# Performance work log

Hardware: AMD Instinct MI355X
Metric: run time of the kernel (lower is better)

The kernel has to match this reference:

```python
import jax, jax.numpy as jnp
import numpy as np

R = 0.01          # slice width (init kwarg r)
DIM = 0           # init kwarg dim = 'x'
NUM_SLICES = 101  # static bound: coords ~ U[0,1) so ceil(range/R) <= 100; +1 safety


def setup_inputs() -> dict:
    key = jax.random.key(0)
    k1, k2 = jax.random.split(key)
    B, N = 16, 65536
    x = jax.random.uniform(k1, (B, 3, N), dtype=jnp.float32)      # point coords in [0,1)
    x_64 = jax.random.normal(k2, (B, 64, N), dtype=jnp.float32)   # per-point features
    return {"x": x, "x_64": x_64, "batch_": B, "points": N}


def reference(x, x_64, batch_, points):
    # per-batch min along the chosen axis: [B]
    pmin = x[:, DIM, :].min(axis=1)
    coord = x[:, DIM, :]                                          # [B, N]
    # bucket index per point (torch.floor((point - min)/r))
    k = jnp.floor((coord - pmin[:, None]) / R).astype(jnp.int32)  # [B, N]
    seg = k.reshape(-1)                                           # [B*N] global slice ids (original pools across batch)
    feats = jnp.transpose(x_64, (0, 2, 1)).reshape(-1, 64)        # [B*N, 64]
    # vectorized segment max replacing the python per-slice loop
    max_feature = jax.ops.segment_max(feats, seg, num_segments=NUM_SLICES)  # [NUM_SLICES, 64]
    counts = jax.ops.segment_sum(jnp.ones_like(seg, dtype=jnp.int32), seg,
                                 num_segments=NUM_SLICES)         # [NUM_SLICES] = slice_num
    return max_feature, counts
```

## Files before the change

### kernel.cpp

```cpp
#include <hip/hip_runtime.h>

#define NSEG 101
#define NCH 64
#define NPTS 65536
#define NBATCH 16
#define NMAX (NCH * NSEG)
#define NOUT (NMAX + NSEG)
#define FLT_BIG 3.4028234663852886e38f

#define SENT 0x007FFFFFu
#define BITS_EMPTY 0xFF7F0000u
#define BITS_POS_CLAMP 0x7F7F0000u

static __device__ __forceinline__ unsigned enc(float f) {
    unsigned b = (unsigned)__float_as_int(f);
    return b ^ (0x80000000u | (unsigned)((int)b >> 31));
}
static __device__ __forceinline__ unsigned dec_bits(unsigned u) {
    unsigned flip = (u & 0x80000000u) ? 0x80000000u : 0xFFFFFFFFu;
    return u ^ flip;
}

__global__ __launch_bounds__(256) void sp4_minp(const float* __restrict__ x,
                                                float* __restrict__ pm_part,
                                                unsigned* __restrict__ acc) {
    int b = blockIdx.x >> 4, ch = blockIdx.x & 15;
    int t = threadIdx.x;

    int e = blockIdx.x * 256 + t;
    if (e < NMAX) acc[e] = SENT;
    else if (e < NOUT) acc[e] = 0u;

    const float4* row = (const float4*)(x + (size_t)b * 3 * NPTS + (size_t)ch * 4096);
    float m = FLT_BIG;
    #pragma unroll
    for (int i = 0; i < 4; i++) {
        float4 v = row[t + i * 256];
        m = fminf(m, fminf(fminf(v.x, v.y), fminf(v.z, v.w)));
    }
    #pragma unroll
    for (int off = 32; off; off >>= 1)
        m = fminf(m, __shfl_down(m, off, 64));
    __shared__ float sm[4];
    if ((t & 63) == 0) sm[t >> 6] = m;
    __syncthreads();
    if (t == 0)
        pm_part[blockIdx.x] = fminf(fminf(sm[0], sm[1]), fminf(sm[2], sm[3]));
}

__global__ void sp4_seed(unsigned* __restrict__ acc) {
    int e = blockIdx.x * 256 + threadIdx.x;
    if (e < NMAX) acc[e] = SENT;
    else if (e < NOUT) acc[e] = 0u;
}

template<bool PMIN_WS>
__global__ __launch_bounds__(512, 4) void sp4_main(const float* __restrict__ x,
                                                   const float* __restrict__ x64,
                                                   const float* __restrict__ pm_part,
                                                   unsigned* __restrict__ acc) {
    __shared__ unsigned smax[NMAX];
    __shared__ unsigned scnt[NSEG];
    int t = threadIdx.x;
    for (int i = t; i < NMAX; i += 512) smax[i] = SENT;
    if (t < NSEG) scnt[t] = 0u;

    int b = blockIdx.x >> 5;
    int chunk = blockIdx.x & 31;

    float pm;
    if constexpr (PMIN_WS) {
        float r = pm_part[b * 16];
        #pragma unroll
        for (int i = 1; i < 16; i++) r = fminf(r, pm_part[b * 16 + i]);
        pm = r;
        __syncthreads();
    } else {
        __shared__ float swmin[8];
        const float4* crow = (const float4*)(x + (size_t)b * 3 * NPTS);
        float m = FLT_BIG;
        #pragma unroll
        for (int i = 0; i < 32; i++) {
            float4 v = crow[t + i * 512];
            m = fminf(m, fminf(fminf(v.x, v.y), fminf(v.z, v.w)));
        }
        #pragma unroll
        for (int off = 32; off; off >>= 1)
            m = fminf(m, __shfl_down(m, off, 64));
        if ((t & 63) == 0) swmin[t >> 6] = m;
        __syncthreads();
        pm = swmin[0];
        #pragma unroll
        for (int i = 1; i < 8; i++) pm = fminf(pm, swmin[i]);
    }

    int n0 = chunk * 2048 + t * 4;
    float4 cv = *(const float4*)(x + (size_t)b * 3 * NPTS + n0);
    int k0 = (int)floorf((cv.x - pm) / 0.01f);
    int k1 = (int)floorf((cv.y - pm) / 0.01f);
    int k2 = (int)floorf((cv.z - pm) / 0.01f);
    int k3 = (int)floorf((cv.w - pm) / 0.01f);
    k0 = k0 < 0 ? 0 : (k0 > NSEG - 1 ? NSEG - 1 : k0);
    k1 = k1 < 0 ? 0 : (k1 > NSEG - 1 ? NSEG - 1 : k1);
    k2 = k2 < 0 ? 0 : (k2 > NSEG - 1 ? NSEG - 1 : k2);
    k3 = k3 < 0 ? 0 : (k3 > NSEG - 1 ? NSEG - 1 : k3);
    atomicAdd(&scnt[k0], 1u);
    atomicAdd(&scnt[k1], 1u);
    atomicAdd(&scnt[k2], 1u);
    atomicAdd(&scnt[k3], 1u);

    const float* gp = x64 + (size_t)b * NCH * NPTS + n0;
    #pragma unroll 8
    for (int c = 0; c < NCH; c++) {
        float4 v = *(const float4*)(gp + (size_t)c * NPTS);
        atomicMax(&smax[c * NSEG + k0], enc(v.x));
        atomicMax(&smax[c * NSEG + k1], enc(v.y));
        atomicMax(&smax[c * NSEG + k2], enc(v.z));
        atomicMax(&smax[c * NSEG + k3], enc(v.w));
    }
    __syncthreads();

    for (int e = t; e < NOUT; e += 512) {
        if (e < NMAX) {
            unsigned v = smax[(e & 63) * NSEG + (e >> 6)];
            if (v != SENT) atomicMax(&acc[e], v);
        } else {
            unsigned v = scnt[e - NMAX];
            if (v) atomicAdd(&acc[e], v);
        }
    }
}

__global__ void sp4_fin(unsigned* __restrict__ acc) {
    int e = blockIdx.x * 256 + threadIdx.x;
    if (e >= NOUT) return;
    unsigned u = acc[e];
    unsigned ob;
    if (e < NMAX) {
        if (u == SENT) {
            ob = BITS_EMPTY;
        } else {
            ob = dec_bits(u);
            unsigned mag = ob & 0x7FFFFFFFu;
            if (mag >= 0x7F7F8000u)
                ob = (ob & 0x80000000u) | BITS_POS_CLAMP;
        }
    } else {
        ob = (unsigned)__float_as_int((float)u);
    }
    acc[e] = ob;
}

extern "C" void kernel_launch(void* const* d_in, const int* in_sizes, int n_in,
                              void* d_out, int out_size, void* d_ws, size_t ws_size,
                              hipStream_t stream) {
    const float* x   = (const float*)d_in[0];
    const float* x64 = (const float*)d_in[1];
    unsigned* acc = (unsigned*)d_out;
    float* pm_part = (float*)d_ws;

    if (ws_size >= 256 * sizeof(float)) {
        sp4_minp<<<256, 256, 0, stream>>>(x, pm_part, acc);
        sp4_main<true><<<NBATCH * 32, 512, 0, stream>>>(x, x64, pm_part, acc);
    } else {
        sp4_seed<<<(NOUT + 255) / 256, 256, 0, stream>>>(acc);
        sp4_main<false><<<NBATCH * 32, 512, 0, stream>>>(x, x64, nullptr, acc);
    }
    sp4_fin<<<(NOUT + 255) / 256, 256, 0, stream>>>(acc);
}
```

Measured before the change: 59.03 us.

## Fuse finalize into main kernel via last-block counter and stagger global atomics

The separate finalize kernel is removed on the workspace path. A global counter lets the last block to finish the main kernel decode the accumulated results in place, using atomic reads for coherence. Each block's flush of its shared-memory maxima to global atomics now starts at a block-dependent offset, which spreads contention across addresses. This saves one kernel launch at the cost of a serial tail run by a single block, plus a threadfence and a counter atomic in every block.

```diff
diff --git a/kernel.cpp b/kernel.cpp
--- a/kernel.cpp
+++ b/kernel.cpp
@@ -20,16 +20,29 @@
     unsigned flip = (u & 0x80000000u) ? 0x80000000u : 0xFFFFFFFFu;
     return u ^ flip;
 }
+static __device__ __forceinline__ unsigned finalize_bits(int e, unsigned u) {
+    if (e < NMAX) {
+        if (u == SENT) return BITS_EMPTY;
+        unsigned ob = dec_bits(u);
+        unsigned mag = ob & 0x7FFFFFFFu;
+        if (mag >= 0x7F7F8000u)
+            ob = (ob & 0x80000000u) | BITS_POS_CLAMP;
+        return ob;
+    }
+    return (unsigned)__float_as_int((float)u);
+}
 
-__global__ __launch_bounds__(256) void sp4_minp(const float* __restrict__ x,
+__global__ __launch_bounds__(256) void sp5_minp(const float* __restrict__ x,
                                                 float* __restrict__ pm_part,
-                                                unsigned* __restrict__ acc) {
+                                                unsigned* __restrict__ acc,
+                                                unsigned* __restrict__ ctr) {
     int b = blockIdx.x >> 4, ch = blockIdx.x & 15;
     int t = threadIdx.x;
 
     int e = blockIdx.x * 256 + t;
     if (e < NMAX) acc[e] = SENT;
     else if (e < NOUT) acc[e] = 0u;
+    if (blockIdx.x == 0 && t == 0) *ctr = 0u;
 
     const float4* row = (const float4*)(x + (size_t)b * 3 * NPTS + (size_t)ch * 4096);
     float m = FLT_BIG;
@@ -48,17 +61,18 @@
         pm_part[blockIdx.x] = fminf(fminf(sm[0], sm[1]), fminf(sm[2], sm[3]));
 }
 
-__global__ void sp4_seed(unsigned* __restrict__ acc) {
+__global__ void sp5_seed(unsigned* __restrict__ acc) {
     int e = blockIdx.x * 256 + threadIdx.x;
     if (e < NMAX) acc[e] = SENT;
     else if (e < NOUT) acc[e] = 0u;
 }
 
-template<bool PMIN_WS>
-__global__ __launch_bounds__(512, 4) void sp4_main(const float* __restrict__ x,
+template<bool FUSE>
+__global__ __launch_bounds__(512, 4) void sp5_main(const float* __restrict__ x,
                                                    const float* __restrict__ x64,
                                                    const float* __restrict__ pm_part,
-                                                   unsigned* __restrict__ acc) {
+                                                   unsigned* __restrict__ acc,
+                                                   unsigned* __restrict__ ctr) {
     __shared__ unsigned smax[NMAX];
     __shared__ unsigned scnt[NSEG];
     int t = threadIdx.x;
@@ -69,7 +83,7 @@
     int chunk = blockIdx.x & 31;
 
     float pm;
-    if constexpr (PMIN_WS) {
+    if constexpr (FUSE) {
         float r = pm_part[b * 16];
         #pragma unroll
         for (int i = 1; i < 16; i++) r = fminf(r, pm_part[b * 16 + i]);
@@ -120,35 +134,37 @@
     }
     __syncthreads();
 
+    int s = (int)((blockIdx.x * 1283u) % NOUT);
     for (int e = t; e < NOUT; e += 512) {
-        if (e < NMAX) {
-            unsigned v = smax[(e & 63) * NSEG + (e >> 6)];
-            if (v != SENT) atomicMax(&acc[e], v);
+        int idx = e + s; if (idx >= NOUT) idx -= NOUT;
+        if (idx < NMAX) {
+            unsigned v = smax[(idx & 63) * NSEG + (idx >> 6)];
+            if (v != SENT) atomicMax(&acc[idx], v);
         } else {
-            unsigned v = scnt[e - NMAX];
-            if (v) atomicAdd(&acc[e], v);
+            unsigned v = scnt[idx - NMAX];
+            if (v) atomicAdd(&acc[idx], v);
+        }
+    }
+
+    if constexpr (FUSE) {
+        __shared__ unsigned s_last;
+        __threadfence();
+        if (t == 0) s_last = (atomicAdd(ctr, 1u) == gridDim.x - 1) ? 1u : 0u;
+        __syncthreads();
+        if (s_last) {
+            for (int e = t; e < NOUT; e += 512) {
+                unsigned u = (e < NMAX) ? atomicMax(&acc[e], 0u)
+                                        : atomicAdd(&acc[e], 0u);
+                acc[e] = finalize_bits(e, u);
+            }
         }
     }
 }
 
-__global__ void sp4_fin(unsigned* __restrict__ acc) {
+__global__ void sp5_fin(unsigned* __restrict__ acc) {
     int e = blockIdx.x * 256 + threadIdx.x;
     if (e >= NOUT) return;
-    unsigned u = acc[e];
-    unsigned ob;
-    if (e < NMAX) {
-        if (u == SENT) {
-            ob = BITS_EMPTY;
-        } else {
-            ob = dec_bits(u);
-            unsigned mag = ob & 0x7FFFFFFFu;
-            if (mag >= 0x7F7F8000u)
-                ob = (ob & 0x80000000u) | BITS_POS_CLAMP;
-        }
-    } else {
-        ob = (unsigned)__float_as_int((float)u);
-    }
-    acc[e] = ob;
+    acc[e] = finalize_bits(e, acc[e]);
 }
 
 extern "C" void kernel_launch(void* const* d_in, const int* in_sizes, int n_in,
@@ -158,13 +174,14 @@
     const float* x64 = (const float*)d_in[1];
     unsigned* acc = (unsigned*)d_out;
     float* pm_part = (float*)d_ws;
+    unsigned* ctr = (unsigned*)((char*)d_ws + 1024);
 
-    if (ws_size >= 256 * sizeof(float)) {
-        sp4_minp<<<256, 256, 0, stream>>>(x, pm_part, acc);
-        sp4_main<true><<<NBATCH * 32, 512, 0, stream>>>(x, x64, pm_part, acc);
+    if (ws_size >= 1024 + sizeof(unsigned)) {
+        sp5_minp<<<256, 256, 0, stream>>>(x, pm_part, acc, ctr);
+        sp5_main<true><<<NBATCH * 32, 512, 0, stream>>>(x, x64, pm_part, acc, ctr);
     } else {
-        sp4_seed<<<(NOUT + 255) / 256, 256, 0, stream>>>(acc);
-        sp4_main<false><<<NBATCH * 32, 512, 0, stream>>>(x, x64, nullptr, acc);
+        sp5_seed<<<(NOUT + 255) / 256, 256, 0, stream>>>(acc);
+        sp5_main<false><<<NBATCH * 32, 512, 0, stream>>>(x, x64, nullptr, acc, nullptr);
+        sp5_fin<<<(NOUT + 255) / 256, 256, 0, stream>>>(acc);
     }
-    sp4_fin<<<(NOUT + 255) / 256, 256, 0, stream>>>(acc);
 }
```

After: 138.1 us. +134.0%, slower.
